# Performance work log

Hardware: AMD Instinct MI355X
Metric: run time of the kernel (lower is better)

The kernel has to match this reference:

```python
import jax, jax.numpy as jnp
import numpy as np

B, S, D, H, KV, HD = 2, 2048, 4096, 32, 8, 128
N_REP = H // KV


def _rope(t, fr, fi):
    # t: [b, s, h, hd]; fr/fi: [s, hd//2] broadcast as [1, s, 1, hd//2]
    t2 = t.reshape(*t.shape[:-1], -1, 2)
    tr, ti = t2[..., 0], t2[..., 1]
    fr = fr[None, :, None, :]
    fi = fi[None, :, None, :]
    orr = tr * fr - fi * ti
    oi = tr * fi + ti * fr
    return jnp.stack([orr, oi], axis=-1).reshape(t.shape)


def setup_inputs() -> dict:
    key = jax.random.key(0)
    ks = jax.random.split(key, 8)
    scale = 0.02
    x = jax.random.normal(ks[0], (B, S, D), jnp.float32)
    wq = jax.random.normal(ks[1], (H * HD, D), jnp.float32) * scale
    wk = jax.random.normal(ks[2], (KV * HD, D), jnp.float32) * scale
    wv = jax.random.normal(ks[3], (KV * HD, D), jnp.float32) * scale
    wo = jax.random.normal(ks[4], (D, H * HD), jnp.float32) * scale
    # rotary frequencies (real/imag parts of freqs_cis)
    t = jnp.arange(S, dtype=jnp.float32)
    inv = 1.0 / (10000.0 ** (jnp.arange(0, HD, 2, dtype=jnp.float32) / HD))
    ang = t[:, None] * inv[None, :]  # [S, HD//2]
    fr, fi = jnp.cos(ang), jnp.sin(ang)
    # causal mask, additive
    mask = jnp.triu(jnp.full((S, S), -1e9, jnp.float32), 1)[None, None]
    cache_k = jnp.zeros((B, S, KV, HD), jnp.float32)
    cache_v = jnp.zeros((B, S, KV, HD), jnp.float32)
    indexes = jnp.arange(S, dtype=jnp.int32)
    cache_indexes = jnp.arange(S, dtype=jnp.int32)
    return dict(x=x, wq=wq, wk=wk, wv=wv, wo=wo, fr=fr, fi=fi, mask=mask,
                cache_k=cache_k, cache_v=cache_v, indexes=indexes,
                cache_indexes=cache_indexes)


def reference(x, wq, wk, wv, wo, fr, fi, mask, cache_k, cache_v, indexes, cache_indexes):
    bsz, seqlen, _ = x.shape
    xq = jnp.einsum('bsd,ed->bse', x, wq).reshape(bsz, seqlen, H, HD)
    xk = jnp.einsum('bsd,ed->bse', x, wk).reshape(bsz, seqlen, KV, HD)
    xv = jnp.einsum('bsd,ed->bse', x, wv).reshape(bsz, seqlen, KV, HD)
    xq = _rope(xq, fr, fi)
    xk = _rope(xk, fr, fi)
    # KV-cache scatter then gather
    cache_k = cache_k.at[:, indexes].set(xk)
    cache_v = cache_v.at[:, indexes].set(xv)
    keys = cache_k[:, cache_indexes]    # [b, kv_len, KV, hd]
    values = cache_v[:, cache_indexes]
    # GQA: repeat_interleave kv heads
    keys = jnp.repeat(keys, N_REP, axis=2)      # [b, kv_len, H, hd]
    values = jnp.repeat(values, N_REP, axis=2)
    q = xq.transpose(0, 2, 1, 3)        # [b, H, s, hd]
    k = keys.transpose(0, 2, 1, 3)      # [b, H, kv, hd]
    v = values.transpose(0, 2, 1, 3)
    scores = jnp.einsum('bhqd,bhkd->bhqk', q, k) / jnp.sqrt(jnp.float32(HD))
    scores = scores + mask
    probs = jax.nn.softmax(scores.astype(jnp.float32), axis=-1).astype(q.dtype)
    out = jnp.einsum('bhqk,bhkd->bhqd', probs, v)
    out = out.transpose(0, 2, 1, 3).reshape(bsz, seqlen, H * HD)
    out = jnp.einsum('bse,de->bsd', out, wo)
    return (out, xk, xv)
```

## Files before the change

kernel.cpp:

```cpp
#include <hip/hip_runtime.h>
#include <hip/hip_bf16.h>


typedef __attribute__((ext_vector_type(8)))  short s8v;
typedef __attribute__((ext_vector_type(4)))  short s4v;
typedef __attribute__((ext_vector_type(4)))  float f4v;
typedef __attribute__((ext_vector_type(16))) float f16v;
typedef __attribute__((ext_vector_type(2)))  float f2v;
typedef __attribute__((ext_vector_type(2))) unsigned int u2v;
typedef __attribute__((ext_vector_type(4))) unsigned int u4v;

typedef __attribute__((address_space(3))) void lds_void;
typedef __attribute__((address_space(1))) void g_void;

#define GLDS16(gp, lp) __builtin_amdgcn_global_load_lds((g_void*)(gp), (lds_void*)(lp), 16, 0, 0)

#define SCL_LOG2 0.12751744f

__device__ __forceinline__ unsigned short f2b(float f) {
  unsigned u = __builtin_bit_cast(unsigned, f);
  u += 0x7fffu + ((u >> 16) & 1u);
  return (unsigned short)(u >> 16);
}
__device__ __forceinline__ unsigned pk2(float a, float b) {
  return (unsigned)f2b(a) | ((unsigned)f2b(b) << 16);
}
__device__ __forceinline__ float b2f(unsigned short h) {
  return __builtin_bit_cast(float, (unsigned)h << 16);
}

__device__ __forceinline__ void mfma32(f4v& d, s8v a, s8v b) {
  asm volatile("v_mfma_f32_16x16x32_bf16 %0, %1, %2, %0" : "+v"(d) : "v"(a), "v"(b));
}
__device__ __forceinline__ void mfma3216(f16v& d, s8v a, s8v b) {
  asm volatile("v_mfma_f32_32x32x16_bf16 %0, %1, %2, %0" : "+v"(d) : "v"(a), "v"(b));
}
__device__ __forceinline__ s4v tr_read(const char* p, int imm) {
  s4v r;
  asm volatile("ds_read_b64_tr_b16 %0, %1 offset:%2"
               : "=v"(r) : "v"((lds_void*)p), "n"(imm));
  return r;
}

__global__ __launch_bounds__(256) void cvt_bf16(const float* __restrict__ s,
                                                unsigned short* __restrict__ d, int n4) {
  const int i = blockIdx.x * 256 + threadIdx.x;
  if (i >= n4) return;
  f4v v = *(const f4v*)(s + (size_t)i * 4);
  u2v r;
  r.x = pk2(v[0], v[1]);
  r.y = pk2(v[2], v[3]);
  *(u2v*)(d + (size_t)i * 4) = r;
}

#define BAR      asm volatile("s_barrier" ::: "memory")
#define WLGKM    do { asm volatile("s_waitcnt lgkmcnt(0)" ::: "memory"); \
                      __builtin_amdgcn_sched_barrier(0); } while (0)
#define WVM8     do { asm volatile("s_waitcnt vmcnt(8)" ::: "memory"); \
                      __builtin_amdgcn_sched_barrier(0); } while (0)

template <int OUTB>
__global__ __launch_bounds__(512, 2) void gemm_bt8(const unsigned short* __restrict__ A,
                                                   const unsigned short* __restrict__ Bp,
                                                   void* __restrict__ Cout,
                                                   int M, int N, int Ks, int Klen,
                                                   int nTiles) {
  __shared__ __align__(16) char smem[131072];
  const int tid = threadIdx.x, lane = tid & 63, wv = tid >> 6;
  const int qi = lane & 15, g = lane >> 4;
  const int wm = wv >> 2, wn = wv & 3;

  const int nwg = gridDim.x, cpx = nwg >> 3;
  const int id = blockIdx.x;
  const int swz = (id & 7) * cpx + (id >> 3);
  const int half = swz / nTiles;
  const int tile = swz - half * nTiles;
  const int kOff = half * Klen;
  const int MT = M >> 8;
  const int m0 = (tile % MT) * 256, n0 = (tile / MT) * 256;
  const int NT = Klen >> 6;

  const int srowo = wv * 8 + (lane >> 3);
  const int scole = ((lane & 7) ^ (lane >> 3)) << 3;
  const size_t rA = (size_t)(m0 + srowo) * Ks + kOff + scole;
  const size_t rB = (size_t)(n0 + srowo) * Ks + kOff + scole;
  char* sdA = smem + wv * 1024;
  char* sdB = smem + 32768 + wv * 1024;

#define STG_A(D, H, KT) do { \
    GLDS16(A + rA + (size_t)((H)*128) * Ks + (size_t)(KT)*64,      sdA + (D)*65536 + (H)*16384); \
    GLDS16(A + rA + (size_t)((H)*128 + 64) * Ks + (size_t)(KT)*64, sdA + (D)*65536 + (H)*16384 + 8192); } while (0)
#define STG_B(D, H, KT) do { \
    GLDS16(Bp + rB + (size_t)((H)*128) * Ks + (size_t)(KT)*64,      sdB + (D)*65536 + (H)*16384); \
    GLDS16(Bp + rB + (size_t)((H)*128 + 64) * Ks + (size_t)(KT)*64, sdB + (D)*65536 + (H)*16384 + 8192); } while (0)

  const int sw = (qi & 7) << 4;
  const char* frA = smem + (wm * 128 + qi) * 128;
  const char* frB = smem + 32768 + (wn * 64 + qi) * 128;

#define RDA4(D, F0) do { _Pragma("unroll") for (int f_ = 0; f_ < 4; ++f_) \
    _Pragma("unroll") for (int k_ = 0; k_ < 2; ++k_) \
      a[(F0) + f_][k_] = *(const s8v*)(frA + (D)*65536 + ((F0) + f_) * 2048 + (((k_ << 6) + (g << 4)) ^ sw)); } while (0)
#define RDB2(D, N0) do { _Pragma("unroll") for (int n_ = 0; n_ < 2; ++n_) \
    _Pragma("unroll") for (int k_ = 0; k_ < 2; ++k_) \
      b[(N0) + n_][k_] = *(const s8v*)(frB + (D)*65536 + ((N0) + n_) * 2048 + (((k_ << 6) + (g << 4)) ^ sw)); } while (0)
#define MQUAD(F0, N0) do { __builtin_amdgcn_s_setprio(1); \
    _Pragma("unroll") for (int f_ = 0; f_ < 4; ++f_) \
    _Pragma("unroll") for (int n_ = 0; n_ < 2; ++n_) \
    _Pragma("unroll") for (int k_ = 0; k_ < 2; ++k_) \
      mfma32(acc[(F0) + f_][(N0) + n_], a[(F0) + f_][k_], b[(N0) + n_][k_]); \
    __builtin_amdgcn_s_setprio(0); } while (0)

  f4v acc[8][4];
#pragma unroll
  for (int i = 0; i < 8; ++i)
#pragma unroll
    for (int j = 0; j < 4; ++j) acc[i][j] = (f4v)0.0f;

  STG_A(0, 0, 0); STG_A(0, 1, 0); STG_B(0, 0, 0); STG_B(0, 1, 0);
  STG_A(1, 0, 1); STG_A(1, 1, 1); STG_B(1, 0, 1); STG_B(1, 1, 1);
  WVM8;
  BAR;

  s8v a[8][2], b[4][2];
#pragma unroll 1
  for (int it = 0; it < NT / 2; ++it) {
    const int t = 2 * it;
    const int k2 = (t + 2 < NT) ? t + 2 : NT - 1;
    const int k3 = (t + 3 < NT) ? t + 3 : NT - 1;
    RDA4(0, 0); RDB2(0, 0);
    WLGKM; MQUAD(0, 0); BAR;
    RDB2(0, 2);
    WLGKM; MQUAD(0, 2); BAR;
    RDA4(0, 4);
    STG_B(0, 0, k2); STG_B(0, 1, k2);
    WLGKM; MQUAD(4, 0); BAR;
    STG_A(0, 0, k2); STG_A(0, 1, k2);
    MQUAD(4, 2);
    WVM8; BAR;
    RDA4(1, 0); RDB2(1, 0);
    WLGKM; MQUAD(0, 0); BAR;
    RDB2(1, 2);
    WLGKM; MQUAD(0, 2); BAR;
    RDA4(1, 4);
    STG_B(1, 0, k3); STG_B(1, 1, k3);
    WLGKM; MQUAD(4, 0); BAR;
    STG_A(1, 0, k3); STG_A(1, 1, k3);
    MQUAD(4, 2);
    WVM8; BAR;
  }

  asm volatile("s_waitcnt vmcnt(0)" ::: "memory");
  asm volatile("s_nop 7\n\ts_nop 7" ::: "memory");
  const int r4 = g * 4;
  if (OUTB) {
    unsigned short* Cb = (unsigned short*)Cout + (size_t)half * M * N;
#pragma unroll
    for (int fm = 0; fm < 8; ++fm)
#pragma unroll
      for (int fn = 0; fn < 4; ++fn)
#pragma unroll
        for (int r = 0; r < 4; ++r)
          Cb[(size_t)(m0 + wm * 128 + fm * 16 + r4 + r) * N + (n0 + wn * 64 + fn * 16 + qi)] =
              f2b(acc[fm][fn][r]);
  } else {
    float* Cf = (float*)Cout;
#pragma unroll
    for (int fm = 0; fm < 8; ++fm)
#pragma unroll
      for (int fn = 0; fn < 4; ++fn)
#pragma unroll
        for (int r = 0; r < 4; ++r)
          Cf[(size_t)(m0 + wm * 128 + fm * 16 + r4 + r) * N + (n0 + wn * 64 + fn * 16 + qi)] =
              acc[fm][fn][r];
  }
}

__global__ __launch_bounds__(256) void rope_scatter(
    const unsigned short* __restrict__ qkvp, const float* __restrict__ fr,
    const float* __restrict__ fi,
    unsigned short* __restrict__ qb, unsigned short* __restrict__ kb,
    unsigned short* __restrict__ vbuf, float* __restrict__ xk, float* __restrict__ xv) {
  const int idx = blockIdx.x * 256 + threadIdx.x;
  const int token = idx / 3072;
  const int col2  = (idx - token * 3072) * 2;
  const int pos   = token & 2047;
  const unsigned u1 = *(const unsigned*)(qkvp + (size_t)token * 6144 + col2);
  const unsigned u2 = *(const unsigned*)(qkvp + 25165824u + (size_t)token * 6144 + col2);
  float v0 = b2f((unsigned short)u1) + b2f((unsigned short)u2);
  float v1 = b2f((unsigned short)(u1 >> 16)) + b2f((unsigned short)(u2 >> 16));
  if (col2 < 4096) {
    const int j = (col2 & 127) >> 1;
    const float cr = fr[pos * 64 + j], ci = fi[pos * 64 + j];
    const float a = (v0 * cr - ci * v1) * SCL_LOG2;
    const float o = (v0 * ci + v1 * cr) * SCL_LOG2;
    *(unsigned*)(qb + (size_t)token * 4096 + col2) = pk2(a, o);
  } else if (col2 < 5120) {
    const int lc = col2 - 4096;
    const int j = (lc & 127) >> 1;
    const float cr = fr[pos * 64 + j], ci = fi[pos * 64 + j];
    const float a = v0 * cr - ci * v1;
    const float o = v0 * ci + v1 * cr;
    *(unsigned*)(kb + (size_t)token * 1024 + lc) = pk2(a, o);
    f2v w; w.x = a; w.y = o;
    *(f2v*)(xk + (size_t)token * 1024 + lc) = w;
  } else {
    const int lc = col2 - 5120;
    *(unsigned*)(vbuf + (size_t)token * 1024 + lc) = pk2(v0, v1);
    f2v w; w.x = v0; w.y = v1;
    *(f2v*)(xv + (size_t)token * 1024 + lc) = w;
  }
}

__global__ __launch_bounds__(256, 2) void attn_fwd(
    const unsigned short* __restrict__ qb, const unsigned short* __restrict__ kb,
    const unsigned short* __restrict__ vb, unsigned short* __restrict__ ao) {
  __shared__ __align__(16) char smem[81920];
  const int tid = threadIdx.x, lane = tid & 63, wv = tid >> 6;
  const int q31 = lane & 31, hi = lane >> 5;
  const int qtb = 15 - blockIdx.x;
  const int h = blockIdx.y, b = blockIdx.z, kvh = h >> 2;
  const int q0 = qtb * 128;
  const int qrow = q0 + wv * 32 + q31;

  s8v qf[8];
  {
    const unsigned short* qp = qb + (size_t)(b * 2048 + qrow) * 4096 + h * 128 + hi * 8;
#pragma unroll
    for (int c = 0; c < 8; ++c) qf[c] = *(const s8v*)(qp + c * 16);
  }

  f16v oacc[4];
#pragma unroll
  for (int i = 0; i < 4; ++i) oacc[i] = (f16v)0.0f;
  float m_run = -3.0e38f, l_run = 0.0f;

  const unsigned short* ksrc[4]; int kdo[4];
#pragma unroll
  for (int j = 0; j < 4; ++j) {
    const int r = wv * 16 + j * 4 + (lane >> 4);
    ksrc[j] = kb + (size_t)(b * 2048 + r) * 1024 + kvh * 128 + (((lane & 15) ^ (r & 15)) << 3);
    kdo[j] = (wv * 16 + j * 4) * 256;
  }
  const unsigned short* vsrc[4]; int vdo[4];
#pragma unroll
  for (int j = 0; j < 4; ++j) {
    const int key = wv * 16 + j * 4 + ((lane & 7) >> 1);
    const int d = ((lane >> 3) & 7) * 16 + (lane & 1) * 8;
    vsrc[j] = vb + (size_t)(b * 2048 + key) * 1024 + kvh * 128 + d;
    vdo[j] = (wv * 32 + j * 8) * 128;
  }

  const int ntiles = 2 * qtb + 2;
  const int my_qmax = q0 + wv * 32 + 31, wq_lo = q0 + wv * 32;

  {
    char* k0d = smem;
    char* k1d = smem + 16384;
    char* v0d = smem + 49152;
#pragma unroll
    for (int j = 0; j < 4; ++j) GLDS16(ksrc[j], k0d + kdo[j]);
#pragma unroll
    for (int j = 0; j < 4; ++j) GLDS16(ksrc[j] + 65536, k1d + kdo[j]);
#pragma unroll
    for (int j = 0; j < 4; ++j) GLDS16(vsrc[j], v0d + vdo[j]);
  }
  asm volatile("s_waitcnt vmcnt(8)" ::: "memory");
  __builtin_amdgcn_sched_barrier(0);
  BAR;

  int kc = 0;
  for (int t = 0; t < ntiles; ++t) {
    const int k0 = t * 64;
    const bool live = (k0 <= my_qmax);
    const char* Kbase = smem + kc * 16384;
    f16v s32a = (f16v)0.0f, s32b = (f16v)0.0f;
    if (live) {
      __builtin_amdgcn_s_setprio(1);
#pragma unroll
      for (int c = 0; c < 8; ++c) {
        const int sl = ((2 * c + hi) ^ (q31 & 15)) << 4;
        s8v kfa = *(const s8v*)(Kbase + q31 * 256 + sl);
        s8v kfb = *(const s8v*)(Kbase + (32 + q31) * 256 + sl);
        mfma3216(s32a, kfa, qf[c]);
        mfma3216(s32b, kfb, qf[c]);
      }
      __builtin_amdgcn_s_setprio(0);
      asm volatile("s_nop 7\n\ts_nop 7\n\ts_nop 7" : "+v"(s32a), "+v"(s32b));
    }
    {
      const int kt2 = (t + 2 < ntiles) ? t + 2 : ntiles - 1;
      char* kd = smem + ((kc >= 1) ? kc - 1 : 2) * 16384;
#pragma unroll
      for (int j = 0; j < 4; ++j) GLDS16(ksrc[j] + (size_t)kt2 * 65536, kd + kdo[j]);
    }
    asm volatile("s_waitcnt vmcnt(4)" ::: "memory");
    __builtin_amdgcn_sched_barrier(0);
    BAR;
    if (live) {
      const char* vbt = smem + 49152 + (t & 1) * 16384 + hi * 2048 +
                        ((lane >> 4) & 1) * 128 + ((lane & 15) << 3);
      s4v tA[8], tB[8];
#pragma unroll
      for (int u = 0; u < 8; ++u) tA[u] = tr_read(vbt, (u >> 1) * 256 + (u & 1) * 1024);

      float p[32];
#pragma unroll
      for (int r = 0; r < 16; ++r) { p[r] = s32a[r]; p[16 + r] = s32b[r]; }
      float tm = -3.0e38f;
      if (k0 + 64 <= wq_lo) {
#pragma unroll
        for (int j = 0; j < 32; ++j) tm = fmaxf(tm, p[j]);
      } else {
#pragma unroll
        for (int j = 0; j < 32; ++j) {
          const int keyg = k0 + (j >> 4) * 32 + (j & 3) + 8 * ((j >> 2) & 3) + 4 * hi;
          p[j] = (keyg <= qrow) ? p[j] : -3.0e38f;
          tm = fmaxf(tm, p[j]);
        }
      }
      tm = fmaxf(tm, __shfl_xor(tm, 32));

      if (!__all(tm - m_run <= 8.0f)) {
        const float m_new = fmaxf(m_run, tm);
        const float al = exp2f(m_run - m_new);
#pragma unroll
        for (int i = 0; i < 4; ++i)
#pragma unroll
          for (int r = 0; r < 16; ++r) oacc[i][r] *= al;
        l_run *= al;
        m_run = m_new;
      }
      float ps = 0.0f;
#pragma unroll
      for (int j = 0; j < 32; ++j) { p[j] = exp2f(p[j] - m_run); ps += p[j]; }
      ps += __shfl_xor(ps, 32);
      l_run += ps;

      s8v pf[4];
#pragma unroll
      for (int ks = 0; ks < 4; ++ks) {
        unsigned c0, c1, c2, c3;
        asm("v_cvt_pk_bf16_f32 %0, %1, %2" : "=v"(c0) : "v"(p[ks*8+0]), "v"(p[ks*8+1]));
        asm("v_cvt_pk_bf16_f32 %0, %1, %2" : "=v"(c1) : "v"(p[ks*8+2]), "v"(p[ks*8+3]));
        asm("v_cvt_pk_bf16_f32 %0, %1, %2" : "=v"(c2) : "v"(p[ks*8+4]), "v"(p[ks*8+5]));
        asm("v_cvt_pk_bf16_f32 %0, %1, %2" : "=v"(c3) : "v"(p[ks*8+6]), "v"(p[ks*8+7]));
        asm volatile("v_permlane32_swap_b32 %0, %1" : "+v"(c0), "+v"(c2));
        asm volatile("v_permlane32_swap_b32 %0, %1" : "+v"(c1), "+v"(c3));
        u4v pw; pw.x = c0; pw.y = c1; pw.z = c2; pw.w = c3;
        pf[ks] = __builtin_bit_cast(s8v, pw);
      }

#define PVS(KS, CUR, NXT, LAST) do { \
        if (!(LAST)) { \
          _Pragma("unroll") for (int u = 0; u < 8; ++u) \
            NXT[u] = tr_read(vbt, ((KS)+1)*4096 + (u >> 1) * 256 + (u & 1) * 1024); \
          asm volatile("s_waitcnt lgkmcnt(8)" ::: "memory"); \
        } else { asm volatile("s_waitcnt lgkmcnt(0)" ::: "memory"); } \
        __builtin_amdgcn_sched_barrier(0); \
        __builtin_amdgcn_s_setprio(1); \
        _Pragma("unroll") for (int dt = 0; dt < 4; ++dt) { \
          s8v vf = __builtin_shufflevector(CUR[dt*2], CUR[dt*2+1], 0,1,2,3,4,5,6,7); \
          mfma3216(oacc[dt], vf, pf[KS]); } \
        __builtin_amdgcn_s_setprio(0); \
      } while (0)
      PVS(0, tA, tB, 0);
      PVS(1, tB, tA, 0);
      PVS(2, tA, tB, 0);
      PVS(3, tB, tA, 1);
#undef PVS
    }
    {
      const int vt1 = (t + 1 < ntiles) ? t + 1 : ntiles - 1;
      char* vd = smem + 49152 + ((t + 1) & 1) * 16384;
#pragma unroll
      for (int j = 0; j < 4; ++j) GLDS16(vsrc[j] + (size_t)vt1 * 65536, vd + vdo[j]);
    }
    kc = (kc == 2) ? 0 : kc + 1;
  }

  asm volatile("s_waitcnt vmcnt(0) lgkmcnt(0)" ::: "memory");
  asm volatile("s_nop 7\n\ts_nop 7\n\ts_nop 7" ::: "memory");
  __syncthreads();
  const float inv = 1.0f / l_run;
  float* Ost = (float*)smem;
  const int er = tid >> 2, ew = (tid & 3) * 32;
#pragma unroll
  for (int p = 0; p < 2; ++p) {
    if ((wv >> 1) == p) {
      const int qip = (wv & 1) * 32 + q31;
#pragma unroll
      for (int dt = 0; dt < 4; ++dt)
#pragma unroll
        for (int r = 0; r < 16; ++r) {
          const int d = dt * 32 + (r & 3) + 8 * ((r >> 2) & 3) + 4 * hi;
          Ost[qip * 128 + (d ^ ((qip & 7) << 2))] = oacc[dt][r] * inv;
        }
    }
    __syncthreads();
    const int sw = (er & 7) << 2;
    f4v av[8];
#pragma unroll
    for (int c = 0; c < 8; ++c)
      av[c] = *(const f4v*)(Ost + er * 128 + ((ew + c * 4) ^ sw));
    u4v r0, r1;
    r0.x = pk2(av[0][0], av[0][1]); r0.y = pk2(av[0][2], av[0][3]);
    r0.z = pk2(av[1][0], av[1][1]); r0.w = pk2(av[1][2], av[1][3]);
    r1.x = pk2(av[2][0], av[2][1]); r1.y = pk2(av[2][2], av[2][3]);
    r1.z = pk2(av[3][0], av[3][1]); r1.w = pk2(av[3][2], av[3][3]);
    u4v r2, r3;
    r2.x = pk2(av[4][0], av[4][1]); r2.y = pk2(av[4][2], av[4][3]);
    r2.z = pk2(av[5][0], av[5][1]); r2.w = pk2(av[5][2], av[5][3]);
    r3.x = pk2(av[6][0], av[6][1]); r3.y = pk2(av[6][2], av[6][3]);
    r3.z = pk2(av[7][0], av[7][1]); r3.w = pk2(av[7][2], av[7][3]);
    unsigned short* dst = ao + (size_t)(b * 2048 + q0 + p * 64 + er) * 4096 + h * 128 + ew;
    *(u4v*)dst = r0;
    *(u4v*)(dst + 8) = r1;
    *(u4v*)(dst + 16) = r2;
    *(u4v*)(dst + 24) = r3;
    __syncthreads();
  }
}

extern "C" void kernel_launch(void* const* d_in, const int* in_sizes, int n_in,
                              void* d_out, int out_size, void* d_ws, size_t ws_size,
                              hipStream_t stream) {
  (void)in_sizes; (void)n_in; (void)out_size; (void)ws_size;
  const float* x  = (const float*)d_in[0];
  const float* wq = (const float*)d_in[1];
  const float* wk = (const float*)d_in[2];
  const float* wv = (const float*)d_in[3];
  const float* wo = (const float*)d_in[4];
  const float* fr = (const float*)d_in[5];
  const float* fi = (const float*)d_in[6];

  float* out = (float*)d_out;
  float* xk  = out + 16777216;
  float* xv  = xk + 4194304;

  char* ws = (char*)d_ws;
  unsigned short* xb    = (unsigned short*)(ws);
  unsigned short* wqkvb = (unsigned short*)(ws + 33554432);
  unsigned short* wob   = (unsigned short*)(ws + 83886080);
  unsigned short* qkvb  = (unsigned short*)(ws + 117440512);
  unsigned short* aob   = (unsigned short*)(ws + 117440512);
  unsigned short* qbuf  = (unsigned short*)(ws + 218103808);
  unsigned short* kbuf  = (unsigned short*)(ws + 251658240);
  unsigned short* vbuf  = (unsigned short*)(ws + 260046848);

  cvt_bf16<<<16384, 256, 0, stream>>>(x,  xb, 4194304);
  cvt_bf16<<<16384, 256, 0, stream>>>(wq, wqkvb, 4194304);
  cvt_bf16<<<4096,  256, 0, stream>>>(wk, wqkvb + 16777216, 1048576);
  cvt_bf16<<<4096,  256, 0, stream>>>(wv, wqkvb + 20971520, 1048576);
  cvt_bf16<<<16384, 256, 0, stream>>>(wo, wob, 4194304);

  gemm_bt8<1><<<768, 512, 0, stream>>>(xb, wqkvb, qkvb, 4096, 6144, 4096, 2048, 384);
  rope_scatter<<<49152, 256, 0, stream>>>(qkvb, fr, fi, qbuf, kbuf, vbuf, xk, xv);
  attn_fwd<<<dim3(16, 32, 2), 256, 0, stream>>>(qbuf, kbuf, vbuf, aob);
  gemm_bt8<0><<<256, 512, 0, stream>>>(aob, wob, out, 4096, 4096, 4096, 4096, 256);
}
```

Baseline: 578.8 us.

## Replace split-K QKV GEMM with dedicated 256x192 full-K kernel

Adds a dedicated QKV projection GEMM that uses 256x192 tiles over the full K dimension, with 512 blocks and double-buffered LDS staging. It replaces the earlier split-K version, which wrote two bf16 partial sums per element. rope_scatter now reads one bf16 value per element instead of adding two partials, and passes V through unchanged. This removes the partial-sum write and read traffic and the extra adds, at the cost of less parallelism per tile and a different tile shape that may change occupancy and LDS use. The attention output buffer is moved to its own workspace region so it no longer aliases the QKV output.

```diff
diff --git a/kernel.cpp b/kernel.cpp
--- a/kernel.cpp
+++ b/kernel.cpp
@@ -58,6 +58,104 @@
                       __builtin_amdgcn_sched_barrier(0); } while (0)
 #define WVM8     do { asm volatile("s_waitcnt vmcnt(8)" ::: "memory"); \
                       __builtin_amdgcn_sched_barrier(0); } while (0)
+#define WVM7     do { asm volatile("s_waitcnt vmcnt(7)" ::: "memory"); \
+                      __builtin_amdgcn_sched_barrier(0); } while (0)
+
+__global__ __launch_bounds__(512, 2) void gemm_qkv(const unsigned short* __restrict__ A,
+                                                   const unsigned short* __restrict__ Bp,
+                                                   unsigned short* __restrict__ C) {
+  __shared__ __align__(16) char smem[114688];
+  const int tid = threadIdx.x, lane = tid & 63, wv = tid >> 6;
+  const int qi = lane & 15, g = lane >> 4;
+  const int wm = wv >> 1, wn = wv & 1;
+  const int K = 4096, N = 6144, NT = 64;
+
+  const int id = blockIdx.x;
+  const int swz = (id & 7) * 64 + (id >> 3);
+  const int m0 = (swz & 15) * 256, n0 = (swz >> 4) * 192;
+
+  const int srowo = wv * 8 + (lane >> 3);
+  const int scole = ((lane & 7) ^ (lane >> 3)) << 3;
+  const size_t rA = (size_t)(m0 + srowo) * K + scole;
+  const size_t rB = (size_t)(n0 + srowo) * K + scole;
+  char* sdA = smem + wv * 1024;
+  char* sdB = smem + 65536 + wv * 1024;
+
+#define QSTG_A(D, KT) do { _Pragma("unroll") for (int c_ = 0; c_ < 4; ++c_) \
+    GLDS16(A + rA + (size_t)(c_ * 64) * K + (size_t)(KT) * 64, \
+           sdA + (D) * 32768 + c_ * 8192); } while (0)
+#define QSTG_B(D, KT) do { _Pragma("unroll") for (int c_ = 0; c_ < 3; ++c_) \
+    GLDS16(Bp + rB + (size_t)(c_ * 64) * K + (size_t)(KT) * 64, \
+           sdB + (D) * 24576 + c_ * 8192); } while (0)
+
+  const int sw = (qi & 7) << 4;
+  const char* frA = smem + (wm * 64 + qi) * 128;
+  const char* frB = smem + 65536 + (wn * 96 + qi) * 128;
+
+#define QRDA(D, F0) do { _Pragma("unroll") for (int f_ = 0; f_ < 2; ++f_) \
+    _Pragma("unroll") for (int k_ = 0; k_ < 2; ++k_) \
+      a[(F0) + f_][k_] = *(const s8v*)(frA + (D) * 32768 + ((F0) + f_) * 2048 + (((k_ << 6) + (g << 4)) ^ sw)); } while (0)
+#define QRDB(D, N0) do { _Pragma("unroll") for (int n_ = 0; n_ < 3; ++n_) \
+    _Pragma("unroll") for (int k_ = 0; k_ < 2; ++k_) \
+      b[(N0) + n_][k_] = *(const s8v*)(frB + (D) * 24576 + ((N0) + n_) * 2048 + (((k_ << 6) + (g << 4)) ^ sw)); } while (0)
+#define QMQUAD(F0, N0) do { __builtin_amdgcn_s_setprio(1); \
+    _Pragma("unroll") for (int f_ = 0; f_ < 2; ++f_) \
+    _Pragma("unroll") for (int n_ = 0; n_ < 3; ++n_) \
+    _Pragma("unroll") for (int k_ = 0; k_ < 2; ++k_) \
+      mfma32(acc[(F0) + f_][(N0) + n_], a[(F0) + f_][k_], b[(N0) + n_][k_]); \
+    __builtin_amdgcn_s_setprio(0); } while (0)
+
+  f4v acc[4][6];
+#pragma unroll
+  for (int i = 0; i < 4; ++i)
+#pragma unroll
+    for (int j = 0; j < 6; ++j) acc[i][j] = (f4v)0.0f;
+
+  QSTG_A(0, 0); QSTG_B(0, 0);
+  QSTG_A(1, 1); QSTG_B(1, 1);
+  WVM7;
+  BAR;
+
+  s8v a[4][2], b[6][2];
+#pragma unroll 1
+  for (int it = 0; it < NT / 2; ++it) {
+    const int t = 2 * it;
+    const int k2 = (t + 2 < NT) ? t + 2 : NT - 1;
+    const int k3 = (t + 3 < NT) ? t + 3 : NT - 1;
+    QRDA(0, 0); QRDB(0, 0);
+    WLGKM; QMQUAD(0, 0); BAR;
+    QRDB(0, 3);
+    WLGKM; QMQUAD(0, 3); BAR;
+    QRDA(0, 2);
+    QSTG_B(0, k2);
+    WLGKM; QMQUAD(2, 0); BAR;
+    QSTG_A(0, k2);
+    QMQUAD(2, 3);
+    WVM7; BAR;
+    QRDA(1, 0); QRDB(1, 0);
+    WLGKM; QMQUAD(0, 0); BAR;
+    QRDB(1, 3);
+    WLGKM; QMQUAD(0, 3); BAR;
+    QRDA(1, 2);
+    QSTG_B(1, k3);
+    WLGKM; QMQUAD(2, 0); BAR;
+    QSTG_A(1, k3);
+    QMQUAD(2, 3);
+    WVM7; BAR;
+  }
+
+  asm volatile("s_waitcnt vmcnt(0)" ::: "memory");
+  asm volatile("s_nop 7\n\ts_nop 7" ::: "memory");
+  const int r4 = g * 4;
+#pragma unroll
+  for (int fm = 0; fm < 4; ++fm)
+#pragma unroll
+    for (int fn = 0; fn < 6; ++fn)
+#pragma unroll
+      for (int r = 0; r < 4; ++r)
+        C[(size_t)(m0 + wm * 64 + fm * 16 + r4 + r) * N + (n0 + wn * 96 + fn * 16 + qi)] =
+            f2b(acc[fm][fn][r]);
+}
 
 template <int OUTB>
 __global__ __launch_bounds__(512, 2) void gemm_bt8(const unsigned short* __restrict__ A,
@@ -186,9 +284,8 @@
   const int col2  = (idx - token * 3072) * 2;
   const int pos   = token & 2047;
   const unsigned u1 = *(const unsigned*)(qkvp + (size_t)token * 6144 + col2);
-  const unsigned u2 = *(const unsigned*)(qkvp + 25165824u + (size_t)token * 6144 + col2);
-  float v0 = b2f((unsigned short)u1) + b2f((unsigned short)u2);
-  float v1 = b2f((unsigned short)(u1 >> 16)) + b2f((unsigned short)(u2 >> 16));
+  float v0 = b2f((unsigned short)u1);
+  float v1 = b2f((unsigned short)(u1 >> 16));
   if (col2 < 4096) {
     const int j = (col2 & 127) >> 1;
     const float cr = fr[pos * 64 + j], ci = fi[pos * 64 + j];
@@ -206,7 +303,7 @@
     *(f2v*)(xk + (size_t)token * 1024 + lc) = w;
   } else {
     const int lc = col2 - 5120;
-    *(unsigned*)(vbuf + (size_t)token * 1024 + lc) = pk2(v0, v1);
+    *(unsigned*)(vbuf + (size_t)token * 1024 + lc) = u1;
     f2v w; w.x = v0; w.y = v1;
     *(f2v*)(xv + (size_t)token * 1024 + lc) = w;
   }
@@ -443,7 +540,7 @@
   unsigned short* wqkvb = (unsigned short*)(ws + 33554432);
   unsigned short* wob   = (unsigned short*)(ws + 83886080);
   unsigned short* qkvb  = (unsigned short*)(ws + 117440512);
-  unsigned short* aob   = (unsigned short*)(ws + 117440512);
+  unsigned short* aob   = (unsigned short*)(ws + 167772160);
   unsigned short* qbuf  = (unsigned short*)(ws + 218103808);
   unsigned short* kbuf  = (unsigned short*)(ws + 251658240);
   unsigned short* vbuf  = (unsigned short*)(ws + 260046848);
@@ -454,7 +551,7 @@
   cvt_bf16<<<4096,  256, 0, stream>>>(wv, wqkvb + 20971520, 1048576);
   cvt_bf16<<<16384, 256, 0, stream>>>(wo, wob, 4194304);
 
-  gemm_bt8<1><<<768, 512, 0, stream>>>(xb, wqkvb, qkvb, 4096, 6144, 4096, 2048, 384);
+  gemm_qkv<<<512, 512, 0, stream>>>(xb, wqkvb, qkvb);
   rope_scatter<<<49152, 256, 0, stream>>>(qkvb, fr, fi, qbuf, kbuf, vbuf, xk, xv);
   attn_fwd<<<dim3(16, 32, 2), 256, 0, stream>>>(qbuf, kbuf, vbuf, aob);
   gemm_bt8<0><<<256, 512, 0, stream>>>(aob, wob, out, 4096, 4096, 4096, 4096, 256);
```

Result: faster. 565.3 us (-2.3%).
